# Kernel tuning notes

Measured on AMD Instinct MI355X. Metric: run time of the kernel, lower is better.

## Reference

```python
import jax, jax.numpy as jnp
import numpy as np

B, N, DIM, DD = 32, 4096, 512, 512
SCALE = DD ** -0.5


def setup_inputs() -> dict:
    key = jax.random.key(0)
    ks = jax.random.split(key, 7)
    return {
        "x": jax.random.normal(ks[0], (B, N, DIM), dtype=jnp.float32),
        "Wq": jax.random.normal(ks[1], (DIM, DD), dtype=jnp.float32) * (DIM ** -0.5),
        "Wk": jax.random.normal(ks[2], (DIM, DD), dtype=jnp.float32) * (DIM ** -0.5),
        "Wv": jax.random.normal(ks[3], (DIM, DD), dtype=jnp.float32) * (DIM ** -0.5),
        "Wr": jax.random.normal(ks[4], (DD, DD), dtype=jnp.float32) * (DD ** -0.5),
        "alpha": jax.random.normal(ks[5], (DD,), dtype=jnp.float32),
        "beta": jax.random.normal(ks[6], (DD,), dtype=jnp.float32),
    }


def reference(x, Wq, Wk, Wv, Wr, alpha, beta):
    # projections: [b, n, d]
    q = jnp.einsum('bni,id->bnd', x, Wq)
    k = jnp.einsum('bni,id->bnd', x, Wk)
    v = jnp.einsum('bni,id->bnd', x, Wv)
    # additive attention over feature dim, pooled over sequence
    alpha_w = jax.nn.softmax(q * alpha * SCALE, axis=-1)
    global_query = jnp.sum(q * alpha_w, axis=1)            # [b, d]
    p = global_query[:, None, :] * k                        # [b, n, d]
    beta_w = jax.nn.softmax(p * beta * SCALE, axis=-1)
    global_key = jnp.sum(p * beta_w, axis=1)                # [b, d]
    kv = global_key[:, None, :] * v                         # [b, n, d]
    out = jnp.einsum('bnd,de->bne', kv, Wr) + q
    return out
```

## Files before the change

kernel.cpp:

```cpp
#include <hip/hip_runtime.h>


typedef __attribute__((ext_vector_type(8))) short short8;
typedef __attribute__((ext_vector_type(4))) float floatx4;
typedef unsigned short u16;
typedef unsigned int u32;

#define SEQ 4096
#define BATCH 32
#define NQK 1024
#define FSCALE 0.044194173824159216f

__device__ __forceinline__ u16 f2bf(float f) {
  u32 u = __float_as_uint(f);
  u += 0x7fffu + ((u >> 16) & 1u);
  return (u16)(u >> 16);
}
__device__ __forceinline__ float bf2f(u16 h) { return __uint_as_float((u32)h << 16); }

__device__ __forceinline__ void g2l16(const void* g, void* l) {
  __builtin_amdgcn_global_load_lds(
      (const __attribute__((address_space(1))) void*)g,
      (__attribute__((address_space(3))) void*)l, 16, 0, 0);
}

__global__ __launch_bounds__(256) void convert_x(const float* __restrict__ x,
                                                 u16* __restrict__ xb) {
  size_t i = ((size_t)blockIdx.x * 256 + threadIdx.x) * 8;
  float4 f0 = *(const float4*)(x + i);
  float4 f1 = *(const float4*)(x + i + 4);
  short8 s;
  s[0] = (short)f2bf(f0.x); s[1] = (short)f2bf(f0.y);
  s[2] = (short)f2bf(f0.z); s[3] = (short)f2bf(f0.w);
  s[4] = (short)f2bf(f1.x); s[5] = (short)f2bf(f1.y);
  s[6] = (short)f2bf(f1.z); s[7] = (short)f2bf(f1.w);
  *(short8*)(xb + i) = s;
}

__global__ void prep_w(const float* __restrict__ Wq, const float* __restrict__ Wk,
                       const float* __restrict__ Wr, u16* __restrict__ Wt,
                       u16* __restrict__ Wrt) {
  int n = blockIdx.x;
  if (n < 1024) {
    const float* W = (n < 512) ? Wq : Wk;
    int col = n & 511;
    for (int kk = threadIdx.x; kk < 512; kk += 256)
      Wt[(size_t)n * 512 + kk] = f2bf(W[(size_t)kk * 512 + col]);
  } else {
    int e = n - 1024;
    for (int d = threadIdx.x; d < 512; d += 256)
      Wrt[(size_t)e * 512 + d] = f2bf(Wr[(size_t)d * 512 + e]);
  }
}

template <int LDA, int LDB, int KTILES>
__device__ __forceinline__ void gemm_core(const u16* __restrict__ A,
                                          const u16* __restrict__ B,
                                          int row0, int col0,
                                          u16* sA, u16* sB,
                                          floatx4 (&acc)[4][4]) {
  const int tid = threadIdx.x;
  const int lane = tid & 63, wv = tid >> 6;
  const int wm = (wv >> 1) * 64, wn = (wv & 1) * 64;
  const int ln = lane & 15;
  const int quad = lane >> 4;
  const int b_row = lane >> 2;
  const int b_kq = (lane & 3) * 8;

  for (int kt = 0; kt < KTILES; ++kt) {
    const int k0 = kt * 32;
    __syncthreads();
#pragma unroll
    for (int c = 0; c < 2; ++c) {
      int chunk = wv * 2 + c;
      int r = chunk * 16 + b_row;
      g2l16(A + (size_t)(row0 + r) * LDA + k0 + b_kq, sA + chunk * 512 + lane * 8);
      g2l16(B + (size_t)(col0 + r) * LDB + k0 + b_kq, sB + chunk * 512 + lane * 8);
    }
    __syncthreads();

    short8 a[4], b[4];
#pragma unroll
    for (int i = 0; i < 4; ++i)
      a[i] = *(const short8*)&sA[(wm + i * 16 + ln) * 32 + quad * 8];
#pragma unroll
    for (int j = 0; j < 4; ++j)
      b[j] = *(const short8*)&sB[(wn + j * 16 + ln) * 32 + quad * 8];
#pragma unroll
    for (int i = 0; i < 4; ++i)
#pragma unroll
      for (int j = 0; j < 4; ++j)
        acc[i][j] = __builtin_amdgcn_mfma_f32_16x16x32_bf16(a[i], b[j], acc[i][j], 0, 0, 0);
  }
}

__global__ __launch_bounds__(256) void gemm_qk(const u16* __restrict__ xb,
                                               const u16* __restrict__ Wt,
                                               u16* __restrict__ qk) {
  __shared__ u16 sA[128 * 32];
  __shared__ u16 sB[128 * 32];
  int bid = blockIdx.y * 8 + blockIdx.x;
  int swz = (bid & 7) * 1024 + (bid >> 3);
  const int row0 = (swz >> 3) * 128;
  const int col0 = (swz & 7) * 128;

  floatx4 acc[4][4] = {};
  gemm_core<512, 512, 16>(xb, Wt, row0, col0, sA, sB, acc);

  const int lane = threadIdx.x & 63, wv = threadIdx.x >> 6;
  const int wm = (wv >> 1) * 64, wn = (wv & 1) * 64;
  const int ln = lane & 15, quad = lane >> 4;
#pragma unroll
  for (int i = 0; i < 4; ++i) {
#pragma unroll
    for (int r = 0; r < 4; ++r) {
      int grow = row0 + wm + i * 16 + quad * 4 + r;
      size_t base = (size_t)grow * NQK + col0 + wn + ln;
#pragma unroll
      for (int j = 0; j < 4; ++j) qk[base + j * 16] = f2bf(acc[i][j][r]);
    }
  }
}

__global__ __launch_bounds__(256) void pool_alpha(const u16* __restrict__ qk,
                                                  const float* __restrict__ alpha,
                                                  float* __restrict__ gq) {
  const int b = blockIdx.y;
  const int lane = threadIdx.x & 63, wv = threadIdx.x >> 6;
  const int slot = blockIdx.x * 4 + wv;
  float a8[8], acc8[8];
#pragma unroll
  for (int j = 0; j < 8; ++j) {
    a8[j] = alpha[lane * 8 + j] * FSCALE;
    acc8[j] = 0.f;
  }
  for (int i = 0; i < 64; ++i) {
    int row = slot * 64 + i;
    const u16* qr = qk + (size_t)(b * SEQ + row) * NQK + lane * 8;
    short8 s = *(const short8*)qr;
    float q[8], t[8];
    float m = -1e30f;
#pragma unroll
    for (int j = 0; j < 8; ++j) {
      q[j] = bf2f((u16)s[j]);
      t[j] = q[j] * a8[j];
      m = fmaxf(m, t[j]);
    }
#pragma unroll
    for (int off = 32; off >= 1; off >>= 1) m = fmaxf(m, __shfl_xor(m, off));
    float sum = 0.f;
    float e[8];
#pragma unroll
    for (int j = 0; j < 8; ++j) {
      e[j] = __expf(t[j] - m);
      sum += e[j];
    }
#pragma unroll
    for (int off = 32; off >= 1; off >>= 1) sum += __shfl_xor(sum, off);
    float inv = 1.f / sum;
#pragma unroll
    for (int j = 0; j < 8; ++j) acc8[j] += q[j] * e[j] * inv;
  }
#pragma unroll
  for (int j = 0; j < 8; ++j) atomicAdd(&gq[b * 512 + lane * 8 + j], acc8[j]);
}

__global__ __launch_bounds__(256) void pool_beta(const u16* __restrict__ qk,
                                                 const float* __restrict__ beta,
                                                 const float* __restrict__ gq,
                                                 float* __restrict__ gk) {
  const int b = blockIdx.y;
  const int lane = threadIdx.x & 63, wv = threadIdx.x >> 6;
  const int slot = blockIdx.x * 4 + wv;
  float b8[8], g8[8], acc8[8];
#pragma unroll
  for (int j = 0; j < 8; ++j) {
    b8[j] = beta[lane * 8 + j] * FSCALE;
    g8[j] = gq[b * 512 + lane * 8 + j];
    acc8[j] = 0.f;
  }
  for (int i = 0; i < 64; ++i) {
    int row = slot * 64 + i;
    const u16* kr = qk + (size_t)(b * SEQ + row) * NQK + 512 + lane * 8;
    short8 s = *(const short8*)kr;
    float p[8], t[8];
    float m = -1e30f;
#pragma unroll
    for (int j = 0; j < 8; ++j) {
      p[j] = g8[j] * bf2f((u16)s[j]);
      t[j] = p[j] * b8[j];
      m = fmaxf(m, t[j]);
    }
#pragma unroll
    for (int off = 32; off >= 1; off >>= 1) m = fmaxf(m, __shfl_xor(m, off));
    float sum = 0.f;
    float e[8];
#pragma unroll
    for (int j = 0; j < 8; ++j) {
      e[j] = __expf(t[j] - m);
      sum += e[j];
    }
#pragma unroll
    for (int off = 32; off >= 1; off >>= 1) sum += __shfl_xor(sum, off);
    float inv = 1.f / sum;
#pragma unroll
    for (int j = 0; j < 8; ++j) acc8[j] += p[j] * e[j] * inv;
  }
#pragma unroll
  for (int j = 0; j < 8; ++j) atomicAdd(&gk[b * 512 + lane * 8 + j], acc8[j]);
}

__global__ void build_vgk(const float* __restrict__ Wv, const float* __restrict__ gk,
                          u16* __restrict__ Vgk) {
  int i = blockIdx.x, b = blockIdx.y;
  const float* gr = gk + b * 512;
  const float* wr = Wv + (size_t)i * 512;
  u16* o = Vgk + ((size_t)b * 512 + i) * 512;
  for (int d = threadIdx.x; d < 512; d += 256) o[d] = f2bf(wr[d] * gr[d]);
}

__global__ __launch_bounds__(256) void gemm_wfin(const u16* __restrict__ Wrt,
                                                 const u16* __restrict__ Vgk,
                                                 const float* __restrict__ Wq,
                                                 u16* __restrict__ Wfin) {
  __shared__ u16 sA[128 * 32];
  __shared__ u16 sB[128 * 32];
  const int b = blockIdx.z;
  const int row0 = blockIdx.y * 128;
  const int col0 = blockIdx.x * 128;
  const u16* Bb = Vgk + (size_t)b * 512 * 512;
  u16* Cb = Wfin + (size_t)b * 512 * 512;

  floatx4 acc[4][4] = {};
  gemm_core<512, 512, 16>(Wrt, Bb, row0, col0, sA, sB, acc);

  const int lane = threadIdx.x & 63, wv = threadIdx.x >> 6;
  const int wm = (wv >> 1) * 64, wn = (wv & 1) * 64;
  const int ln = lane & 15, quad = lane >> 4;
#pragma unroll
  for (int i = 0; i < 4; ++i) {
#pragma unroll
    for (int r = 0; r < 4; ++r) {
      int grow = row0 + wm + i * 16 + quad * 4 + r;
#pragma unroll
      for (int j = 0; j < 4; ++j) {
        int gcol = col0 + wn + ln + j * 16;
        Cb[(size_t)grow * 512 + gcol] = f2bf(acc[i][j][r] + Wq[(size_t)gcol * 512 + grow]);
      }
    }
  }
}

__global__ __launch_bounds__(256) void gemm_final(const u16* __restrict__ xb,
                                                  const u16* __restrict__ Wfin,
                                                  float* __restrict__ out) {
  __shared__ u16 sA[128 * 32];
  __shared__ u16 sB[128 * 32];
  const int b = blockIdx.z;
  int bid = blockIdx.y * 4 + blockIdx.x;
  int swz = (bid & 7) * 16 + (bid >> 3);
  const int row0 = (swz >> 2) * 128;
  const int col0 = (swz & 3) * 128;
  const u16* Ab = xb + (size_t)b * SEQ * 512;
  const u16* Bb = Wfin + (size_t)b * 512 * 512;

  floatx4 acc[4][4] = {};
  gemm_core<512, 512, 16>(Ab, Bb, row0, col0, sA, sB, acc);

  const int lane = threadIdx.x & 63, wv = threadIdx.x >> 6;
  const int wm = (wv >> 1) * 64, wn = (wv & 1) * 64;
  const int ln = lane & 15, quad = lane >> 4;
#pragma unroll
  for (int i = 0; i < 4; ++i) {
#pragma unroll
    for (int r = 0; r < 4; ++r) {
      int grow = row0 + wm + i * 16 + quad * 4 + r;
      size_t orow = ((size_t)b * SEQ + grow) * 512;
#pragma unroll
      for (int j = 0; j < 4; ++j) {
        int gcol = col0 + wn + ln + j * 16;
        out[orow + gcol] = acc[i][j][r];
      }
    }
  }
}

extern "C" void kernel_launch(void* const* d_in, const int* in_sizes, int n_in,
                              void* d_out, int out_size, void* d_ws, size_t ws_size,
                              hipStream_t stream) {
  const float* x = (const float*)d_in[0];
  const float* Wq = (const float*)d_in[1];
  const float* Wk = (const float*)d_in[2];
  const float* Wv = (const float*)d_in[3];
  const float* Wr = (const float*)d_in[4];
  const float* alpha = (const float*)d_in[5];
  const float* beta = (const float*)d_in[6];
  float* out = (float*)d_out;

  char* ws = (char*)d_ws;
  u16* xb = (u16*)ws;
  u16* qk = (u16*)(ws + 134217728ull);
  u16* Vgk = (u16*)(ws + 134217728ull);
  u16* Wfin = (u16*)(ws + 151994944ull);
  u16* Wt = (u16*)(ws + 402653184ull);
  u16* Wrt = (u16*)(ws + 403701760ull);
  float* gq = (float*)(ws + 404226048ull);
  float* gk = gq + 16384;

  hipMemsetAsync(gq, 0, 131072, stream);
  convert_x<<<32768, 256, 0, stream>>>(x, xb);
  prep_w<<<1536, 256, 0, stream>>>(Wq, Wk, Wr, Wt, Wrt);
  gemm_qk<<<dim3(8, 1024), 256, 0, stream>>>(xb, Wt, qk);
  pool_alpha<<<dim3(16, BATCH), 256, 0, stream>>>(qk, alpha, gq);
  pool_beta<<<dim3(16, BATCH), 256, 0, stream>>>(qk, beta, gq, gk);
  build_vgk<<<dim3(512, BATCH), 256, 0, stream>>>(Wv, gk, Vgk);
  gemm_wfin<<<dim3(4, 4, BATCH), 256, 0, stream>>>(Wrt, Vgk, Wq, Wfin);
  gemm_final<<<dim3(4, 32, BATCH), 256, 0, stream>>>(xb, Wfin, out);
}
```

Baseline: 1.042 ms.

## Double-buffer LDS tiles in shared GEMM core to overlap loads with MFMA

The GEMM core now uses two LDS buffers for the A and B tiles. The next K-tile is issued with global_load_lds while the current tile is fed to MFMA, and only one barrier is needed per tile instead of two. Global pointer offsets are precomputed outside the loop. This is meant to hide global-to-LDS latency behind compute, at the cost of double the LDS per block, which may reduce occupancy.

After: 983.9 us. 1.06x faster.

```diff
diff --git a/kernel.cpp b/kernel.cpp
--- a/kernel.cpp
+++ b/kernel.cpp
@@ -57,7 +57,7 @@
 __device__ __forceinline__ void gemm_core(const u16* __restrict__ A,
                                           const u16* __restrict__ B,
                                           int row0, int col0,
-                                          u16* sA, u16* sB,
+                                          u16* sA0, u16* sB0, u16* sA1, u16* sB1,
                                           floatx4 (&acc)[4][4]) {
   const int tid = threadIdx.x;
   const int lane = tid & 63, wv = tid >> 6;
@@ -67,45 +67,67 @@
   const int b_row = lane >> 2;
   const int b_kq = (lane & 3) * 8;
 
-  for (int kt = 0; kt < KTILES; ++kt) {
-    const int k0 = kt * 32;
+  const int chunk0 = wv * 2, chunk1 = wv * 2 + 1;
+  const u16* gA0 = A + (size_t)(row0 + chunk0 * 16 + b_row) * LDA + b_kq;
+  const u16* gA1 = A + (size_t)(row0 + chunk1 * 16 + b_row) * LDA + b_kq;
+  const u16* gB0 = B + (size_t)(col0 + chunk0 * 16 + b_row) * LDB + b_kq;
+  const u16* gB1 = B + (size_t)(col0 + chunk1 * 16 + b_row) * LDB + b_kq;
+  const int lA0 = chunk0 * 512 + lane * 8;
+  const int lA1 = chunk1 * 512 + lane * 8;
+
+#define STAGE_KT(pA, pB, kt)                \
+  do {                                      \
+    const int k0_ = (kt) * 32;              \
+    g2l16(gA0 + k0_, (pA) + lA0);           \
+    g2l16(gA1 + k0_, (pA) + lA1);           \
+    g2l16(gB0 + k0_, (pB) + lA0);           \
+    g2l16(gB1 + k0_, (pB) + lA1);           \
+  } while (0)
+
+#define COMPUTE_KT(cA, cB)                                                     \
+  do {                                                                         \
+    short8 a_[4], b_[4];                                                       \
+    _Pragma("unroll") for (int i = 0; i < 4; ++i)                              \
+        a_[i] = *(const short8*)&(cA)[(wm + i * 16 + ln) * 32 + quad * 8];     \
+    _Pragma("unroll") for (int j = 0; j < 4; ++j)                              \
+        b_[j] = *(const short8*)&(cB)[(wn + j * 16 + ln) * 32 + quad * 8];     \
+    _Pragma("unroll") for (int i = 0; i < 4; ++i)                              \
+        _Pragma("unroll") for (int j = 0; j < 4; ++j)                          \
+            acc[i][j] =                                                        \
+        __builtin_amdgcn_mfma_f32_16x16x32_bf16(a_[i], b_[j], acc[i][j], 0, 0, 0); \
+  } while (0)
+
+  STAGE_KT(sA0, sB0, 0);
+  __syncthreads();
+
+  for (int kt = 0; kt < KTILES; kt += 2) {
+    STAGE_KT(sA1, sB1, kt + 1);
+    COMPUTE_KT(sA0, sB0);
     __syncthreads();
-#pragma unroll
-    for (int c = 0; c < 2; ++c) {
-      int chunk = wv * 2 + c;
-      int r = chunk * 16 + b_row;
-      g2l16(A + (size_t)(row0 + r) * LDA + k0 + b_kq, sA + chunk * 512 + lane * 8);
-      g2l16(B + (size_t)(col0 + r) * LDB + k0 + b_kq, sB + chunk * 512 + lane * 8);
-    }
-    __syncthreads();
-
-    short8 a[4], b[4];
-#pragma unroll
-    for (int i = 0; i < 4; ++i)
-      a[i] = *(const short8*)&sA[(wm + i * 16 + ln) * 32 + quad * 8];
-#pragma unroll
-    for (int j = 0; j < 4; ++j)
-      b[j] = *(const short8*)&sB[(wn + j * 16 + ln) * 32 + quad * 8];
-#pragma unroll
-    for (int i = 0; i < 4; ++i)
-#pragma unroll
-      for (int j = 0; j < 4; ++j)
-        acc[i][j] = __builtin_amdgcn_mfma_f32_16x16x32_bf16(a[i], b[j], acc[i][j], 0, 0, 0);
-  }
+
+    if (kt + 2 < KTILES) {
+      STAGE_KT(sA0, sB0, kt + 2);
+      COMPUTE_KT(sA1, sB1);
+      __syncthreads();
+    } else {
+      COMPUTE_KT(sA1, sB1);
+    }
+  }
+#undef STAGE_KT
+#undef COMPUTE_KT
 }
 
 __global__ __launch_bounds__(256) void gemm_qk(const u16* __restrict__ xb,
                                                const u16* __restrict__ Wt,
                                                u16* __restrict__ qk) {
-  __shared__ u16 sA[128 * 32];
-  __shared__ u16 sB[128 * 32];
+  __shared__ u16 sA0[128 * 32], sB0[128 * 32], sA1[128 * 32], sB1[128 * 32];
   int bid = blockIdx.y * 8 + blockIdx.x;
   int swz = (bid & 7) * 1024 + (bid >> 3);
   const int row0 = (swz >> 3) * 128;
   const int col0 = (swz & 7) * 128;
 
   floatx4 acc[4][4] = {};
-  gemm_core<512, 512, 16>(xb, Wt, row0, col0, sA, sB, acc);
+  gemm_core<512, 512, 16>(xb, Wt, row0, col0, sA0, sB0, sA1, sB1, acc);
 
   const int lane = threadIdx.x & 63, wv = threadIdx.x >> 6;
   const int wm = (wv >> 1) * 64, wn = (wv & 1) * 64;
@@ -223,8 +245,7 @@
                                                  const u16* __restrict__ Vgk,
                                                  const float* __restrict__ Wq,
                                                  u16* __restrict__ Wfin) {
-  __shared__ u16 sA[128 * 32];
-  __shared__ u16 sB[128 * 32];
+  __shared__ u16 sA0[128 * 32], sB0[128 * 32], sA1[128 * 32], sB1[128 * 32];
   const int b = blockIdx.z;
   const int row0 = blockIdx.y * 128;
   const int col0 = blockIdx.x * 128;
@@ -232,7 +253,7 @@
   u16* Cb = Wfin + (size_t)b * 512 * 512;
 
   floatx4 acc[4][4] = {};
-  gemm_core<512, 512, 16>(Wrt, Bb, row0, col0, sA, sB, acc);
+  gemm_core<512, 512, 16>(Wrt, Bb, row0, col0, sA0, sB0, sA1, sB1, acc);
 
   const int lane = threadIdx.x & 63, wv = threadIdx.x >> 6;
   const int wm = (wv >> 1) * 64, wn = (wv & 1) * 64;
@@ -254,8 +275,7 @@
 __global__ __launch_bounds__(256) void gemm_final(const u16* __restrict__ xb,
                                                   const u16* __restrict__ Wfin,
                                                   float* __restrict__ out) {
-  __shared__ u16 sA[128 * 32];
-  __shared__ u16 sB[128 * 32];
+  __shared__ u16 sA0[128 * 32], sB0[128 * 32], sA1[128 * 32], sB1[128 * 32];
   const int b = blockIdx.z;
   int bid = blockIdx.y * 4 + blockIdx.x;
   int swz = (bid & 7) * 16 + (bid >> 3);
@@ -265,7 +285,7 @@
   const u16* Bb = Wfin + (size_t)b * 512 * 512;
 
   floatx4 acc[4][4] = {};
-  gemm_core<512, 512, 16>(Ab, Bb, row0, col0, sA, sB, acc);
+  gemm_core<512, 512, 16>(Ab, Bb, row0, col0, sA0, sB0, sA1, sB1, acc);
 
   const int lane = threadIdx.x & 63, wv = threadIdx.x >> 6;
   const int wm = (wv >> 1) * 64, wn = (wv & 1) * 64;
```
